# Kernel optimization log

Measured on AMD Instinct MI355X. Metric: run time of the kernel, lower is better.

Reference implementation:

```python
import jax, jax.numpy as jnp
import numpy as np

B, T, C = 8, 1024, 768
NH = 12
HD = C // NH  # 64


def setup_inputs() -> dict:
    key = jax.random.key(0)
    k1, k2, k3 = jax.random.split(key, 3)
    x = jax.random.normal(k1, (B, T, C), dtype=jnp.float32)
    w_attn = jax.random.normal(k2, (C, 3 * C), dtype=jnp.float32) * 0.02
    b_attn = jnp.zeros((3 * C,), dtype=jnp.float32)
    w_proj = jax.random.normal(k3, (C, C), dtype=jnp.float32) * 0.02
    b_proj = jnp.zeros((C,), dtype=jnp.float32)
    return {"x": x, "w_attn": w_attn, "b_attn": b_attn, "w_proj": w_proj, "b_proj": b_proj}


def reference(x, w_attn, b_attn, w_proj, b_proj):
    Bb, Tt, Cc = x.shape
    qkv = x @ w_attn + b_attn  # [B,T,3C]
    q, k, v = jnp.split(qkv, [Cc, 2 * Cc], axis=-1)
    # [B, NH, T, HD]
    q = q.reshape(Bb, Tt, NH, HD).swapaxes(1, 2)
    k = k.reshape(Bb, Tt, NH, HD).swapaxes(1, 2)
    v = v.reshape(Bb, Tt, NH, HD).swapaxes(1, 2)
    scale = 1.0 / jnp.sqrt(jnp.asarray(HD, dtype=x.dtype))
    att = jnp.einsum("bhqd,bhkd->bhqk", q, k) * scale  # [B,NH,T,T]
    causal = jnp.tril(jnp.ones((Tt, Tt), dtype=bool))[None, None]
    att = jnp.where(causal, att, jnp.asarray(-jnp.inf, dtype=att.dtype))
    att = jax.nn.softmax(att, axis=-1)
    y = jnp.einsum("bhqk,bhkd->bhqd", att, v)  # [B,NH,T,HD]
    y = y.swapaxes(1, 2).reshape(Bb, Tt, Cc)
    return y @ w_proj + b_proj
```

## Files before the change

### kernel.cpp

```cpp
#include <hip/hip_runtime.h>
#include <cstdint>
#include <cstddef>

typedef __attribute__((ext_vector_type(8))) short short8;
typedef __attribute__((ext_vector_type(4))) float f32x4;
typedef __attribute__((ext_vector_type(4))) unsigned short u16x4;

#define ASYNC16(gp, lp) \
  __builtin_amdgcn_global_load_lds((const __attribute__((address_space(1))) unsigned int*)(gp), \
                                   (__attribute__((address_space(3))) unsigned int*)(lp), 16, 0, 0)

__device__ __forceinline__ unsigned short f2b(float f) {
  union { float f; unsigned int u; } c; c.f = f;
  unsigned int u = c.u;
  return (unsigned short)((u + 0x7fffu + ((u >> 16) & 1u)) >> 16);
}


__global__ __launch_bounds__(256) void prep(
    const float* __restrict__ x, unsigned short* __restrict__ xb,
    const float* __restrict__ w_attn, unsigned short* __restrict__ waT,
    const float* __restrict__ w_proj, unsigned short* __restrict__ wpT) {
  __shared__ unsigned short Ts[64][65];
  const int bb = blockIdx.x;
  const int tid = threadIdx.x;
  if (bb < 3072) {
    int i = (bb * 256 + tid) * 8;
    const float* px = x + i;
    short8 v;
    for (int e = 0; e < 8; ++e) ((unsigned short*)&v)[e] = f2b(px[e]);
    *(short8*)(xb + i) = v;
    return;
  }
  const float* W; unsigned short* WT; int Kd, Nd, n0, k0;
  if (bb < 3504) {
    int t = bb - 3072; W = w_attn; WT = waT; Kd = 768; Nd = 2304;
    n0 = (t % 36) * 64; k0 = (t / 36) * 64;
  } else {
    int t = bb - 3504; W = w_proj; WT = wpT; Kd = 768; Nd = 768;
    n0 = (t % 12) * 64; k0 = (t / 12) * 64;
  }
  for (int idx = tid; idx < 4096; idx += 256) {
    int lr = idx >> 6, lc = idx & 63;
    Ts[lr][lc] = f2b(W[(size_t)(k0 + lr) * Nd + n0 + lc]);
  }
  __syncthreads();
  for (int idx = tid; idx < 4096; idx += 256) {
    int nr = idx >> 6, kc = idx & 63;
    WT[(size_t)(n0 + nr) * Kd + k0 + kc] = Ts[kc][nr];
  }
}


__global__ __launch_bounds__(256, 2) void gemm_qkv(
    const unsigned short* __restrict__ A,
    const unsigned short* __restrict__ Bt,
    const float* __restrict__ bias,
    unsigned short* __restrict__ q,
    unsigned short* __restrict__ k,
    unsigned short* __restrict__ vT)
{
  __shared__ unsigned short As[2][128 * 64];
  __shared__ unsigned short Bs[2][128 * 64];
  const int tid = threadIdx.x;
  const int w = tid >> 6, lane = tid & 63;
  const int wm = w >> 1, wn = w & 1;
  const int lr = lane & 15, lq = lane >> 4;

  const int bid = blockIdx.x;
  const int xcd = bid & 7;
  const int local = bid >> 3;
  const int ty = local >> 3;
  const int tx = xcd * 8 + (local & 7);
  const int m0 = tx * 128, n0 = ty * 128;
  const f32x4 fzero = {0.f, 0.f, 0.f, 0.f};

  f32x4 acc[4][4];
  for (int i = 0; i < 4; ++i) for (int j = 0; j < 4; ++j) acc[i][j] = fzero;

  const int trow = tid >> 3;
  const int tcol = (tid & 7) ^ (trow & 7);
  const unsigned short* Asrc = A + (size_t)(m0 + trow) * 768 + tcol * 8;
  const unsigned short* Bsrc = Bt + (size_t)(n0 + trow) * 768 + tcol * 8;
  const int dst0 = tid * 16;

#define STAGE_QKV(s, bidx) do { \
    const unsigned short* as_ = Asrc + (s) * 64; \
    const unsigned short* bs_ = Bsrc + (s) * 64; \
    ASYNC16(as_,            (char*)As[bidx] + dst0); \
    ASYNC16(as_ + 32 * 768, (char*)As[bidx] + dst0 + 4096); \
    ASYNC16(as_ + 64 * 768, (char*)As[bidx] + dst0 + 8192); \
    ASYNC16(as_ + 96 * 768, (char*)As[bidx] + dst0 + 12288); \
    ASYNC16(bs_,            (char*)Bs[bidx] + dst0); \
    ASYNC16(bs_ + 32 * 768, (char*)Bs[bidx] + dst0 + 4096); \
    ASYNC16(bs_ + 64 * 768, (char*)Bs[bidx] + dst0 + 8192); \
    ASYNC16(bs_ + 96 * 768, (char*)Bs[bidx] + dst0 + 12288); \
  } while (0)

  STAGE_QKV(0, 0);

  const int swz = (lq ^ (lr & 7)) * 16;
  const int arow = (wm * 64 + lr) * 128;
  const int brow = (wn * 64 + lr) * 128;

  for (int s = 0; s < 12; ++s) {
    __builtin_amdgcn_s_barrier();
    if (s + 1 < 12) {
      STAGE_QKV(s + 1, (s + 1) & 1);
      asm volatile("s_waitcnt vmcnt(8)" ::: "memory");
    } else {
      asm volatile("s_waitcnt vmcnt(0)" ::: "memory");
    }
    __builtin_amdgcn_s_barrier();
    __builtin_amdgcn_sched_barrier(0);
    const char* asb = (const char*)As[s & 1];
    const char* bsb = (const char*)Bs[s & 1];
    for (int ks = 0; ks < 2; ++ks) {
      const int cb = swz ^ (ks << 6);
      short8 a[4], b[4];
      for (int i = 0; i < 4; ++i)
        a[i] = *(const short8*)(asb + arow + i * 2048 + cb);
      for (int j = 0; j < 4; ++j)
        b[j] = *(const short8*)(bsb + brow + j * 2048 + cb);
      for (int i = 0; i < 4; ++i)
        for (int j = 0; j < 4; ++j)
          acc[i][j] = __builtin_amdgcn_mfma_f32_16x16x32_bf16(a[i], b[j], acc[i][j], 0, 0, 0);
    }
  }
#undef STAGE_QKV

  const int colbase = n0 + wn * 64;
  const int sec = colbase / 768;
  const float QSCALE = 0.18033688011112042f;
  for (int j = 0; j < 4; ++j) {
    int col = colbase + j * 16 + lr;
    int cc = col - sec * 768;
    int h = cc >> 6, d = cc & 63;
    float bv = bias[col];
    for (int i = 0; i < 4; ++i) {
      int row0 = m0 + wm * 64 + i * 16 + lq * 4;
      int bidx = row0 >> 10, t0 = row0 & 1023;
      int bh = bidx * 12 + h;
      if (sec == 0) {
        for (int r = 0; r < 4; ++r)
          q[((size_t)bh * 1024 + t0 + r) * 64 + d] = f2b((acc[i][j][r] + bv) * QSCALE);
      } else if (sec == 1) {
        for (int r = 0; r < 4; ++r)
          k[((size_t)bh * 1024 + t0 + r) * 64 + d] = f2b(acc[i][j][r] + bv);
      } else {
        u16x4 pv;
        pv[0] = f2b(acc[i][j][0] + bv);
        pv[1] = f2b(acc[i][j][1] + bv);
        pv[2] = f2b(acc[i][j][2] + bv);
        pv[3] = f2b(acc[i][j][3] + bv);
        *(u16x4*)(vT + ((size_t)bh * 64 + d) * 1024 + t0) = pv;
      }
    }
  }
}


__global__ __launch_bounds__(256, 3) void attn(
    const unsigned short* __restrict__ q,
    const unsigned short* __restrict__ kk,
    const unsigned short* __restrict__ vT,
    unsigned short* __restrict__ y)
{
  __shared__ unsigned short Qs[128 * 72];
  __shared__ unsigned short Ks[64 * 72];
  __shared__ unsigned short Vt[64 * 72];
  __shared__ unsigned short Ps[4 * 16 * 72];

  const int tid = threadIdx.x;
  const int w = tid >> 6, lane = tid & 63;
  const int lr = lane & 15, lq = lane >> 4;

  const int bid = blockIdx.x;
  const int xcd = bid & 7;
  const int local = bid >> 3;
  const int bh = xcd + 8 * (local >> 3);
  const int qp = local & 7;
  const int qt1 = 15 - qp;
  const int b = bh / 12, h = bh - b * 12;
  const f32x4 fzero = {0.f, 0.f, 0.f, 0.f};

  unsigned short* Pw = Ps + w * 16 * 72;
  const unsigned short* kbase = kk + (size_t)bh * 65536;
  const unsigned short* vbase = vT + (size_t)bh * 65536;

  {
    const unsigned short* qa = q + ((size_t)bh * 1024 + qp * 64) * 64;
    const unsigned short* qb = q + ((size_t)bh * 1024 + qt1 * 64) * 64;
    for (int c = tid; c < 512; c += 256) {
      int row = c >> 3, d0 = (c & 7) * 8;
      *(short8*)(Qs + row * 72 + d0)        = *(const short8*)(qa + (size_t)c * 8);
      *(short8*)(Qs + (row + 64) * 72 + d0) = *(const short8*)(qb + (size_t)c * 8);
    }
  }
  __syncthreads();
  short8 qf0[2], qf1[2];
  for (int ks = 0; ks < 2; ++ks) {
    qf0[ks] = *(const short8*)(Qs + (w * 16 + lr) * 72 + ks * 32 + lq * 8);
    qf1[ks] = *(const short8*)(Qs + (64 + w * 16 + lr) * 72 + ks * 32 + lq * 8);
  }

  const int c0 = tid, c1 = tid + 256;
  short8 kreg[2], vreg[2];
  kreg[0] = *(const short8*)(kbase + (size_t)c0 * 8);
  kreg[1] = *(const short8*)(kbase + (size_t)c1 * 8);
  vreg[0] = *(const short8*)(vbase + (size_t)(c0 >> 3) * 1024 + (c0 & 7) * 8);
  vreg[1] = *(const short8*)(vbase + (size_t)(c1 >> 3) * 1024 + (c1 & 7) * 8);

  f32x4 o0[4], o1[4];
  float l0[4], l1[4];
  for (int jd = 0; jd < 4; ++jd) { o0[jd] = fzero; o1[jd] = fzero; }
  for (int r = 0; r < 4; ++r) { l0[r] = 0.0f; l1[r] = 0.0f; }

  const int nkt = qt1 + 1;

  for (int kt = 0; kt < nkt; ++kt) {
    __syncthreads();
    *(short8*)(Ks + (c0 >> 3) * 72 + (c0 & 7) * 8) = kreg[0];
    *(short8*)(Ks + (c1 >> 3) * 72 + (c1 & 7) * 8) = kreg[1];
    *(short8*)(Vt + (c0 >> 3) * 72 + (c0 & 7) * 8) = vreg[0];
    *(short8*)(Vt + (c1 >> 3) * 72 + (c1 & 7) * 8) = vreg[1];
    __syncthreads();
    if (kt + 1 < nkt) {
      const unsigned short* kp = kbase + (size_t)(kt + 1) * 4096;
      const unsigned short* vp = vbase + (size_t)(kt + 1) * 64;
      kreg[0] = *(const short8*)(kp + (size_t)c0 * 8);
      kreg[1] = *(const short8*)(kp + (size_t)c1 * 8);
      vreg[0] = *(const short8*)(vp + (size_t)(c0 >> 3) * 1024 + (c0 & 7) * 8);
      vreg[1] = *(const short8*)(vp + (size_t)(c1 >> 3) * 1024 + (c1 & 7) * 8);
    }

    short8 bk[2][4];
    for (int ks = 0; ks < 2; ++ks)
      for (int j = 0; j < 4; ++j)
        bk[ks][j] = *(const short8*)(Ks + (j * 16 + lr) * 72 + ks * 32 + lq * 8);

    if (kt <= qp) {
      f32x4 s[4];
      for (int j = 0; j < 4; ++j) s[j] = fzero;
      __builtin_amdgcn_s_setprio(1);
      for (int ks = 0; ks < 2; ++ks) {
        for (int j = 0; j < 4; ++j)
          s[j] = __builtin_amdgcn_mfma_f32_16x16x32_bf16(qf0[ks], bk[ks][j], s[j], 0, 0, 0);
      }
      __builtin_amdgcn_s_setprio(0);
      if (kt == qp) {
        int rowt = w * 16 + lq * 4;
        for (int j = 0; j < 4; ++j) {
          int colt = j * 16 + lr;
          for (int r = 0; r < 4; ++r)
            if (colt > rowt + r) s[j][r] = -1e30f;
        }
      }
      for (int r = 0; r < 4; ++r) {
        int prow = (lq * 4 + r) * 72;
        float acc = 0.0f;
        for (int j = 0; j < 4; ++j) {
          float p = __builtin_amdgcn_exp2f(s[j][r]);
          acc += p;
          union { float f; unsigned int u; } cv; cv.f = p;
          Pw[prow + j * 16 + lr] = (unsigned short)((cv.u + 0x8000u) >> 16);
        }
        l0[r] += acc;
      }
      __builtin_amdgcn_s_setprio(1);
      for (int ks = 0; ks < 2; ++ks) {
        short8 ap = *(const short8*)(Pw + lr * 72 + ks * 32 + lq * 8);
        short8 bv[4];
        for (int jd = 0; jd < 4; ++jd)
          bv[jd] = *(const short8*)(Vt + (jd * 16 + lr) * 72 + ks * 32 + lq * 8);
        for (int jd = 0; jd < 4; ++jd)
          o0[jd] = __builtin_amdgcn_mfma_f32_16x16x32_bf16(ap, bv[jd], o0[jd], 0, 0, 0);
      }
      __builtin_amdgcn_s_setprio(0);
    }

    {
      f32x4 s[4];
      for (int j = 0; j < 4; ++j) s[j] = fzero;
      __builtin_amdgcn_s_setprio(1);
      for (int ks = 0; ks < 2; ++ks) {
        for (int j = 0; j < 4; ++j)
          s[j] = __builtin_amdgcn_mfma_f32_16x16x32_bf16(qf1[ks], bk[ks][j], s[j], 0, 0, 0);
      }
      __builtin_amdgcn_s_setprio(0);
      if (kt == qt1) {
        int rowt = w * 16 + lq * 4;
        for (int j = 0; j < 4; ++j) {
          int colt = j * 16 + lr;
          for (int r = 0; r < 4; ++r)
            if (colt > rowt + r) s[j][r] = -1e30f;
        }
      }
      for (int r = 0; r < 4; ++r) {
        int prow = (lq * 4 + r) * 72;
        float acc = 0.0f;
        for (int j = 0; j < 4; ++j) {
          float p = __builtin_amdgcn_exp2f(s[j][r]);
          acc += p;
          union { float f; unsigned int u; } cv; cv.f = p;
          Pw[prow + j * 16 + lr] = (unsigned short)((cv.u + 0x8000u) >> 16);
        }
        l1[r] += acc;
      }
      __builtin_amdgcn_s_setprio(1);
      for (int ks = 0; ks < 2; ++ks) {
        short8 ap = *(const short8*)(Pw + lr * 72 + ks * 32 + lq * 8);
        short8 bv[4];
        for (int jd = 0; jd < 4; ++jd)
          bv[jd] = *(const short8*)(Vt + (jd * 16 + lr) * 72 + ks * 32 + lq * 8);
        for (int jd = 0; jd < 4; ++jd)
          o1[jd] = __builtin_amdgcn_mfma_f32_16x16x32_bf16(ap, bv[jd], o1[jd], 0, 0, 0);
      }
      __builtin_amdgcn_s_setprio(0);
    }
  }

  for (int r = 0; r < 4; ++r) {
    float a0 = l0[r], a1 = l1[r];
    for (int off = 1; off < 16; off <<= 1) {
      a0 += __shfl_xor(a0, off, 16);
      a1 += __shfl_xor(a1, off, 16);
    }
    l0[r] = 1.0f / a0;
    l1[r] = 1.0f / a1;
  }
  int t0 = qp * 64 + w * 16 + lq * 4;
  int t1 = qt1 * 64 + w * 16 + lq * 4;
  for (int jd = 0; jd < 4; ++jd) {
    int d = jd * 16 + lr;
    for (int r = 0; r < 4; ++r) {
      y[((size_t)b * 1024 + t0 + r) * 768 + h * 64 + d] = f2b(o0[jd][r] * l0[r]);
      y[((size_t)b * 1024 + t1 + r) * 768 + h * 64 + d] = f2b(o1[jd][r] * l1[r]);
    }
  }
}


__global__ __launch_bounds__(256, 3) void gemm_proj(
    const unsigned short* __restrict__ A,
    const unsigned short* __restrict__ Bt,
    const float* __restrict__ bias,
    float* __restrict__ out)
{
  __shared__ unsigned short As[2][64 * 64];
  __shared__ unsigned short Bs[2][128 * 64];
  const int tid = threadIdx.x;
  const int w = tid >> 6, lane = tid & 63;
  const int wm = w >> 1, wn = w & 1;
  const int lr = lane & 15, lq = lane >> 4;

  const int bid = blockIdx.x;
  const int xcd = bid & 7;
  const int local = bid >> 3;
  const int ty = local >> 4;
  const int tx = xcd * 16 + (local & 15);
  const int m0 = tx * 64, n0 = ty * 128;
  const f32x4 fzero = {0.f, 0.f, 0.f, 0.f};

  f32x4 acc[2][4];
  for (int i = 0; i < 2; ++i) for (int j = 0; j < 4; ++j) acc[i][j] = fzero;

  const int trow = tid >> 3;
  const int tcol = (tid & 7) ^ (trow & 7);
  const unsigned short* Asrc = A + (size_t)(m0 + trow) * 768 + tcol * 8;
  const unsigned short* Bsrc = Bt + (size_t)(n0 + trow) * 768 + tcol * 8;
  const int dst0 = tid * 16;

#define STAGE_PROJ(s, bidx) do { \
    const unsigned short* as_ = Asrc + (s) * 64; \
    const unsigned short* bs_ = Bsrc + (s) * 64; \
    ASYNC16(as_,            (char*)As[bidx] + dst0); \
    ASYNC16(as_ + 32 * 768, (char*)As[bidx] + dst0 + 4096); \
    ASYNC16(bs_,            (char*)Bs[bidx] + dst0); \
    ASYNC16(bs_ + 32 * 768, (char*)Bs[bidx] + dst0 + 4096); \
    ASYNC16(bs_ + 64 * 768, (char*)Bs[bidx] + dst0 + 8192); \
    ASYNC16(bs_ + 96 * 768, (char*)Bs[bidx] + dst0 + 12288); \
  } while (0)

  STAGE_PROJ(0, 0);

  const int swz = (lq ^ (lr & 7)) * 16;
  const int arow = (wm * 32 + lr) * 128;
  const int brow = (wn * 64 + lr) * 128;

  for (int s = 0; s < 12; ++s) {
    __builtin_amdgcn_s_barrier();
    if (s + 1 < 12) {
      STAGE_PROJ(s + 1, (s + 1) & 1);
      asm volatile("s_waitcnt vmcnt(6)" ::: "memory");
    } else {
      asm volatile("s_waitcnt vmcnt(0)" ::: "memory");
    }
    __builtin_amdgcn_s_barrier();
    __builtin_amdgcn_sched_barrier(0);
    const char* asb = (const char*)As[s & 1];
    const char* bsb = (const char*)Bs[s & 1];
    for (int ks = 0; ks < 2; ++ks) {
      const int cb = swz ^ (ks << 6);
      short8 a[2], b[4];
      for (int i = 0; i < 2; ++i)
        a[i] = *(const short8*)(asb + arow + i * 2048 + cb);
      for (int j = 0; j < 4; ++j)
        b[j] = *(const short8*)(bsb + brow + j * 2048 + cb);
      for (int i = 0; i < 2; ++i)
        for (int j = 0; j < 4; ++j)
          acc[i][j] = __builtin_amdgcn_mfma_f32_16x16x32_bf16(a[i], b[j], acc[i][j], 0, 0, 0);
    }
  }
#undef STAGE_PROJ

  for (int j = 0; j < 4; ++j) {
    int col = n0 + wn * 64 + j * 16 + lr;
    float bv = bias[col];
    for (int i = 0; i < 2; ++i) {
      int row0 = m0 + wm * 32 + i * 16 + lq * 4;
      for (int r = 0; r < 4; ++r)
        out[(size_t)(row0 + r) * 768 + col] = acc[i][j][r] + bv;
    }
  }
}


extern "C" void kernel_launch(void* const* d_in, const int* in_sizes, int n_in,
                              void* d_out, int out_size, void* d_ws, size_t ws_size,
                              hipStream_t stream) {
  const float* x      = (const float*)d_in[0];
  const float* w_attn = (const float*)d_in[1];
  const float* b_attn = (const float*)d_in[2];
  const float* w_proj = (const float*)d_in[3];
  const float* b_proj = (const float*)d_in[4];
  float* out = (float*)d_out;

  char* p = (char*)d_ws;
  unsigned short* xb  = (unsigned short*)p; p += (size_t)8192 * 768 * 2;
  unsigned short* waT = (unsigned short*)p; p += (size_t)2304 * 768 * 2;
  unsigned short* wpT = (unsigned short*)p; p += (size_t)768 * 768 * 2;
  unsigned short* qb  = (unsigned short*)p; p += (size_t)96 * 1024 * 64 * 2;
  unsigned short* kb  = (unsigned short*)p; p += (size_t)96 * 1024 * 64 * 2;
  unsigned short* vTb = (unsigned short*)p; p += (size_t)96 * 64 * 1024 * 2;
  unsigned short* yb  = (unsigned short*)p; p += (size_t)8192 * 768 * 2;

  prep<<<3648, 256, 0, stream>>>(x, xb, w_attn, waT, w_proj, wpT);
  gemm_qkv<<<1152, 256, 0, stream>>>(xb, waT, b_attn, qb, kb, vTb);
  attn<<<768, 256, 0, stream>>>(qb, kb, vTb, yb);
  gemm_proj<<<768, 256, 0, stream>>>(yb, wpT, b_proj, out);
}
```

Before: 176.6 us.

## Use triple-buffered 32-wide K tiles with single barrier in QKV GEMM

Restructures the QKV GEMM main loop from double-buffered 64-wide K stages to triple-buffered 32-wide stages with prefetch distance two and one barrier per iteration. LDS per block shrinks, so launch bounds are raised to allow three blocks per CU. The aim is better latency hiding and occupancy, at the cost of twice as many loop iterations and barriers and a new swizzle pattern.

```diff
diff --git a/kernel.cpp b/kernel.cpp
--- a/kernel.cpp
+++ b/kernel.cpp
@@ -52,7 +52,7 @@
 }
 
 
-__global__ __launch_bounds__(256, 2) void gemm_qkv(
+__global__ __launch_bounds__(256, 3) void gemm_qkv(
     const unsigned short* __restrict__ A,
     const unsigned short* __restrict__ Bt,
     const float* __restrict__ bias,
@@ -60,8 +60,8 @@
     unsigned short* __restrict__ k,
     unsigned short* __restrict__ vT)
 {
-  __shared__ unsigned short As[2][128 * 64];
-  __shared__ unsigned short Bs[2][128 * 64];
+  __shared__ unsigned short As[3][128 * 32];
+  __shared__ unsigned short Bs[3][128 * 32];
   const int tid = threadIdx.x;
   const int w = tid >> 6, lane = tid & 63;
   const int wm = w >> 1, wn = w & 1;
@@ -78,54 +78,49 @@
   f32x4 acc[4][4];
   for (int i = 0; i < 4; ++i) for (int j = 0; j < 4; ++j) acc[i][j] = fzero;
 
-  const int trow = tid >> 3;
-  const int tcol = (tid & 7) ^ (trow & 7);
-  const unsigned short* Asrc = A + (size_t)(m0 + trow) * 768 + tcol * 8;
-  const unsigned short* Bsrc = Bt + (size_t)(n0 + trow) * 768 + tcol * 8;
+  const int trow = tid >> 2;
+  const int gc = (tid & 3) ^ ((tid >> 3) & 3);
+  const unsigned short* Asrc = A + (size_t)(m0 + trow) * 768 + gc * 8;
+  const unsigned short* Bsrc = Bt + (size_t)(n0 + trow) * 768 + gc * 8;
   const int dst0 = tid * 16;
 
 #define STAGE_QKV(s, bidx) do { \
-    const unsigned short* as_ = Asrc + (s) * 64; \
-    const unsigned short* bs_ = Bsrc + (s) * 64; \
+    const unsigned short* as_ = Asrc + (s) * 32; \
+    const unsigned short* bs_ = Bsrc + (s) * 32; \
     ASYNC16(as_,            (char*)As[bidx] + dst0); \
-    ASYNC16(as_ + 32 * 768, (char*)As[bidx] + dst0 + 4096); \
-    ASYNC16(as_ + 64 * 768, (char*)As[bidx] + dst0 + 8192); \
-    ASYNC16(as_ + 96 * 768, (char*)As[bidx] + dst0 + 12288); \
+    ASYNC16(as_ + 64 * 768, (char*)As[bidx] + dst0 + 4096); \
     ASYNC16(bs_,            (char*)Bs[bidx] + dst0); \
-    ASYNC16(bs_ + 32 * 768, (char*)Bs[bidx] + dst0 + 4096); \
-    ASYNC16(bs_ + 64 * 768, (char*)Bs[bidx] + dst0 + 8192); \
-    ASYNC16(bs_ + 96 * 768, (char*)Bs[bidx] + dst0 + 12288); \
+    ASYNC16(bs_ + 64 * 768, (char*)Bs[bidx] + dst0 + 4096); \
   } while (0)
 
   STAGE_QKV(0, 0);
-
-  const int swz = (lq ^ (lr & 7)) * 16;
-  const int arow = (wm * 64 + lr) * 128;
-  const int brow = (wn * 64 + lr) * 128;
-
-  for (int s = 0; s < 12; ++s) {
-    __builtin_amdgcn_s_barrier();
-    if (s + 1 < 12) {
-      STAGE_QKV(s + 1, (s + 1) & 1);
-      asm volatile("s_waitcnt vmcnt(8)" ::: "memory");
-    } else {
-      asm volatile("s_waitcnt vmcnt(0)" ::: "memory");
-    }
+  STAGE_QKV(1, 1);
+
+  const int swz = (lq ^ ((lr >> 1) & 3)) * 16;
+  const int arow = (wm * 64 + lr) * 64;
+  const int brow = (wn * 64 + lr) * 64;
+
+  int bi = 0;
+  for (int s = 0; s < 24; ++s) {
+    if (s < 23) asm volatile("s_waitcnt vmcnt(4)" ::: "memory");
+    else        asm volatile("s_waitcnt vmcnt(0)" ::: "memory");
     __builtin_amdgcn_s_barrier();
     __builtin_amdgcn_sched_barrier(0);
-    const char* asb = (const char*)As[s & 1];
-    const char* bsb = (const char*)Bs[s & 1];
-    for (int ks = 0; ks < 2; ++ks) {
-      const int cb = swz ^ (ks << 6);
-      short8 a[4], b[4];
-      for (int i = 0; i < 4; ++i)
-        a[i] = *(const short8*)(asb + arow + i * 2048 + cb);
+    if (s + 2 < 24) {
+      int b2 = bi + 2; if (b2 >= 3) b2 -= 3;
+      STAGE_QKV(s + 2, b2);
+    }
+    const char* asb = (const char*)As[bi];
+    const char* bsb = (const char*)Bs[bi];
+    short8 a[4], b[4];
+    for (int i = 0; i < 4; ++i)
+      a[i] = *(const short8*)(asb + arow + i * 1024 + swz);
+    for (int j = 0; j < 4; ++j)
+      b[j] = *(const short8*)(bsb + brow + j * 1024 + swz);
+    for (int i = 0; i < 4; ++i)
       for (int j = 0; j < 4; ++j)
-        b[j] = *(const short8*)(bsb + brow + j * 2048 + cb);
-      for (int i = 0; i < 4; ++i)
-        for (int j = 0; j < 4; ++j)
-          acc[i][j] = __builtin_amdgcn_mfma_f32_16x16x32_bf16(a[i], b[j], acc[i][j], 0, 0, 0);
-    }
+        acc[i][j] = __builtin_amdgcn_mfma_f32_16x16x32_bf16(a[i], b[j], acc[i][j], 0, 0, 0);
+    ++bi; if (bi == 3) bi = 0;
   }
 #undef STAGE_QKV
 
```

After: 181.0 us. 1.02x slower.

## Double-buffer K/V tiles in LDS to drop one barrier per iteration

Applied to the files above, without the earlier changes.

The attention kernel now keeps two LDS buffers each for K and V and aliases the Q staging area onto them in one shared pool. Each iteration writes the next tile into the alternate buffer and prefetches the tile after that into registers. This drops one of the two __syncthreads per key tile and moves the initial K/V global loads ahead of the Q load. The cost is more LDS (about 45 KB), which could limit occupancy at three blocks per CU, and the remaining single barrier must still protect buffer reuse.

```diff
diff --git a/kernel.cpp b/kernel.cpp
--- a/kernel.cpp
+++ b/kernel.cpp
@@ -166,10 +166,13 @@
     const unsigned short* __restrict__ vT,
     unsigned short* __restrict__ y)
 {
-  __shared__ unsigned short Qs[128 * 72];
-  __shared__ unsigned short Ks[64 * 72];
-  __shared__ unsigned short Vt[64 * 72];
-  __shared__ unsigned short Ps[4 * 16 * 72];
+  __shared__ __attribute__((aligned(16))) char smem[46080];
+  unsigned short* KsB0 = (unsigned short*)smem;
+  unsigned short* KsB1 = (unsigned short*)(smem + 9216);
+  unsigned short* VtB0 = (unsigned short*)(smem + 18432);
+  unsigned short* VtB1 = (unsigned short*)(smem + 27648);
+  unsigned short* Ps   = (unsigned short*)(smem + 36864);
+  unsigned short* Qs   = (unsigned short*)smem;
 
   const int tid = threadIdx.x;
   const int w = tid >> 6, lane = tid & 63;
@@ -188,6 +191,13 @@
   const unsigned short* kbase = kk + (size_t)bh * 65536;
   const unsigned short* vbase = vT + (size_t)bh * 65536;
 
+  const int c0 = tid, c1 = tid + 256;
+  short8 kreg[2], vreg[2];
+  kreg[0] = *(const short8*)(kbase + (size_t)c0 * 8);
+  kreg[1] = *(const short8*)(kbase + (size_t)c1 * 8);
+  vreg[0] = *(const short8*)(vbase + (size_t)(c0 >> 3) * 1024 + (c0 & 7) * 8);
+  vreg[1] = *(const short8*)(vbase + (size_t)(c1 >> 3) * 1024 + (c1 & 7) * 8);
+
   {
     const unsigned short* qa = q + ((size_t)bh * 1024 + qp * 64) * 64;
     const unsigned short* qb = q + ((size_t)bh * 1024 + qt1 * 64) * 64;
@@ -203,35 +213,50 @@
     qf0[ks] = *(const short8*)(Qs + (w * 16 + lr) * 72 + ks * 32 + lq * 8);
     qf1[ks] = *(const short8*)(Qs + (64 + w * 16 + lr) * 72 + ks * 32 + lq * 8);
   }
-
-  const int c0 = tid, c1 = tid + 256;
-  short8 kreg[2], vreg[2];
-  kreg[0] = *(const short8*)(kbase + (size_t)c0 * 8);
-  kreg[1] = *(const short8*)(kbase + (size_t)c1 * 8);
-  vreg[0] = *(const short8*)(vbase + (size_t)(c0 >> 3) * 1024 + (c0 & 7) * 8);
-  vreg[1] = *(const short8*)(vbase + (size_t)(c1 >> 3) * 1024 + (c1 & 7) * 8);
+  __syncthreads();
+
+  const int wo0 = (c0 >> 3) * 72 + (c0 & 7) * 8;
+  const int wo1 = (c1 >> 3) * 72 + (c1 & 7) * 8;
+
+  *(short8*)(KsB0 + wo0) = kreg[0];
+  *(short8*)(KsB0 + wo1) = kreg[1];
+  *(short8*)(VtB0 + wo0) = vreg[0];
+  *(short8*)(VtB0 + wo1) = vreg[1];
+
+  const int nkt = qt1 + 1;
+  {
+    const unsigned short* kp = kbase + 4096;
+    const unsigned short* vp = vbase + 64;
+    kreg[0] = *(const short8*)(kp + (size_t)c0 * 8);
+    kreg[1] = *(const short8*)(kp + (size_t)c1 * 8);
+    vreg[0] = *(const short8*)(vp + (size_t)(c0 >> 3) * 1024 + (c0 & 7) * 8);
+    vreg[1] = *(const short8*)(vp + (size_t)(c1 >> 3) * 1024 + (c1 & 7) * 8);
+  }
 
   f32x4 o0[4], o1[4];
   float l0[4], l1[4];
   for (int jd = 0; jd < 4; ++jd) { o0[jd] = fzero; o1[jd] = fzero; }
   for (int r = 0; r < 4; ++r) { l0[r] = 0.0f; l1[r] = 0.0f; }
 
-  const int nkt = qt1 + 1;
-
   for (int kt = 0; kt < nkt; ++kt) {
     __syncthreads();
-    *(short8*)(Ks + (c0 >> 3) * 72 + (c0 & 7) * 8) = kreg[0];
-    *(short8*)(Ks + (c1 >> 3) * 72 + (c1 & 7) * 8) = kreg[1];
-    *(short8*)(Vt + (c0 >> 3) * 72 + (c0 & 7) * 8) = vreg[0];
-    *(short8*)(Vt + (c1 >> 3) * 72 + (c1 & 7) * 8) = vreg[1];
-    __syncthreads();
+    const unsigned short* Ks = (kt & 1) ? KsB1 : KsB0;
+    const unsigned short* Vt = (kt & 1) ? VtB1 : VtB0;
     if (kt + 1 < nkt) {
-      const unsigned short* kp = kbase + (size_t)(kt + 1) * 4096;
-      const unsigned short* vp = vbase + (size_t)(kt + 1) * 64;
-      kreg[0] = *(const short8*)(kp + (size_t)c0 * 8);
-      kreg[1] = *(const short8*)(kp + (size_t)c1 * 8);
-      vreg[0] = *(const short8*)(vp + (size_t)(c0 >> 3) * 1024 + (c0 & 7) * 8);
-      vreg[1] = *(const short8*)(vp + (size_t)(c1 >> 3) * 1024 + (c1 & 7) * 8);
+      unsigned short* Ksn = (kt & 1) ? KsB0 : KsB1;
+      unsigned short* Vtn = (kt & 1) ? VtB0 : VtB1;
+      *(short8*)(Ksn + wo0) = kreg[0];
+      *(short8*)(Ksn + wo1) = kreg[1];
+      *(short8*)(Vtn + wo0) = vreg[0];
+      *(short8*)(Vtn + wo1) = vreg[1];
+      if (kt + 2 < nkt) {
+        const unsigned short* kp = kbase + (size_t)(kt + 2) * 4096;
+        const unsigned short* vp = vbase + (size_t)(kt + 2) * 64;
+        kreg[0] = *(const short8*)(kp + (size_t)c0 * 8);
+        kreg[1] = *(const short8*)(kp + (size_t)c1 * 8);
+        vreg[0] = *(const short8*)(vp + (size_t)(c0 >> 3) * 1024 + (c0 & 7) * 8);
+        vreg[1] = *(const short8*)(vp + (size_t)(c1 >> 3) * 1024 + (c1 & 7) * 8);
+      }
     }
 
     short8 bk[2][4];
```

Measured after the change: 172.4 us. 2.4% less time.
